# Kernel optimization log

Measured on AMD Instinct MI355X. Metric: run time of the kernel, lower is better.

## Reference

```python
import jax, jax.numpy as jnp
import numpy as np

ALPHA = 1.8   # Levy stability index (undefined global in source; chosen heavy-tailed)
BETA = 0.0    # symmetric
SIGMA = 0.5
DEPTH = 25
DIM = 64
HID = 100
BATCH = 262144


def _levy_noise(u_raw, w_raw):
    """Chambers-Mallows-Stuck sampler for symmetric alpha-stable (beta=0).
    u_raw, w_raw ~ U(0,1); returns clipped noise, scale=0.1, clamp [-10,10]."""
    U = jnp.pi * (u_raw - 0.5)                       # U(-pi/2, pi/2)
    W = -jnp.log(jnp.clip(w_raw, 1e-12, 1.0))        # Exp(1)
    inv_a = 1.0 / ALPHA
    X = (jnp.sin(ALPHA * U) / jnp.cos(U) ** inv_a) * \
        (jnp.cos(U - ALPHA * U) / jnp.clip(W, 1e-12, None)) ** ((1.0 - ALPHA) * inv_a)
    return jnp.clip(0.1 * X, -10.0, 10.0)


def setup_inputs() -> dict:
    key = jax.random.key(0)
    ks = jax.random.split(key, 8)
    d, h = DIM, HID
    return {
        "x": jax.random.normal(ks[0], (BATCH, d), dtype=jnp.float32),
        "u_raw": jax.random.uniform(ks[1], (DEPTH, d), dtype=jnp.float32),
        "w_raw": jax.random.uniform(ks[2], (DEPTH, d), dtype=jnp.float32),
        "W_down": jax.random.normal(ks[3], (d, d), dtype=jnp.float32) / np.sqrt(d),
        "b_down": jnp.zeros((d,), jnp.float32),
        "W_drift": jax.random.normal(ks[4], (d, d), dtype=jnp.float32) / np.sqrt(d),
        "b_drift": jnp.zeros((d,), jnp.float32),
        "W1": jax.random.normal(ks[5], (d, h), dtype=jnp.float32) / np.sqrt(d),
        "b1": jnp.zeros((h,), jnp.float32),
        "W2": jax.random.normal(ks[6], (h, 1), dtype=jnp.float32) / np.sqrt(h),
        "b2": jnp.zeros((1,), jnp.float32),
    }


def reference(x, u_raw, w_raw, W_down, b_down, W_drift, b_drift, W1, b1, W2, b2):
    dt = 1.0 / DEPTH
    out = x @ W_down + b_down                                   # [B, d]
    # diffusion logit on the INITIAL state, held fixed through the loop
    logit = jax.nn.relu(out @ W1 + b1) @ W2 + b2                # [B, 1]
    scale = SIGMA * jax.nn.sigmoid(logit) * dt ** (1.0 / ALPHA)  # [B, 1]
    noise = _levy_noise(u_raw, w_raw)                           # [DEPTH, d]

    def step(out, n):
        drift = jax.nn.relu(out @ W_drift + b_drift) + out      # DriftNet: relu(lin)+x
        return out + drift * dt + scale * n, None

    out, _ = jax.lax.scan(step, out, noise)
    drift_out = jax.nn.relu(out @ W_drift + b_drift) + out
    return drift_out, out
```

## Files before the change

### kernel.cpp

```cpp
#include <hip/hip_runtime.h>

#define DEPTH 25
#define DIM   64
#define HID   100

typedef _Float16 f16x4 __attribute__((ext_vector_type(4)));
typedef _Float16 f16x8 __attribute__((ext_vector_type(8)));
typedef __fp16   h2    __attribute__((ext_vector_type(2)));
typedef float    f32x4 __attribute__((ext_vector_type(4)));
typedef float    f32x2 __attribute__((ext_vector_type(2)));

__global__ __launch_bounds__(64) void levy_noise_kernel(
    const float* __restrict__ u_raw, const float* __restrict__ w_raw,
    float* __restrict__ noise)
{
    const int idx = blockIdx.x * 64 + threadIdx.x;
    if (idx >= DEPTH * DIM) return;
    float u = u_raw[idx];
    float w = w_raw[idx];
    float U  = 3.14159265358979323846f * (u - 0.5f);
    float Wv = -logf(fminf(fmaxf(w, 1e-12f), 1.0f));
    float t1 = sinf(1.8f * U) / powf(cosf(U), 0.5555555555555556f);
    float ratio = cosf(0.8f * U) / fmaxf(Wv, 1e-12f);
    float X = t1 * powf(ratio, -0.4444444444444444f);
    noise[idx] = fminf(fmaxf(0.1f * X, -10.0f), 10.0f);
}

__global__ __launch_bounds__(256) void preconv_kernel(
    const float* __restrict__ W_down, const float* __restrict__ W_drift,
    const float* __restrict__ W1,     const float* __restrict__ b1,
    const float* __restrict__ W2,
    _Float16* __restrict__ wpre, float* __restrict__ b1p, float* __restrict__ w2p)
{
    const int idx = blockIdx.x * 256 + threadIdx.x;
    if (idx < 7680) {
        int rel, kind;
        if (idx < 2048)      { kind = 0; rel = idx; }
        else if (idx < 4096) { kind = 1; rel = idx - 2048; }
        else                 { kind = 2; rel = idx - 4096; }
        const int fi    = rel >> 8;
        const int lane2 = (rel >> 2) & 63;
        const int j     = (rel & 3) * 2;
        const int m     = (fi >> 1) * 16 + (lane2 & 15);
        const int k     = (fi & 1) * 32 + ((j & 4) ? 16 : 0)
                        + (lane2 >> 4) * 4 + (j & 3);
        float v0, v1;
        if (kind == 0) {
            v0 = W_down[k * DIM + m];           v1 = W_down[(k + 1) * DIM + m];
        } else if (kind == 1) {
            v0 = 0.04f * W_drift[k * DIM + m];  v1 = 0.04f * W_drift[(k + 1) * DIM + m];
        } else {
            v0 = (m < HID) ? W1[k * HID + m] : 0.0f;
            v1 = (m < HID) ? W1[(k + 1) * HID + m] : 0.0f;
        }
        *(h2*)(wpre + idx * 2) = __builtin_amdgcn_cvt_pkrtz(v0, v1);
    } else if (idx < 7792) {
        const int i = idx - 7680;
        b1p[i] = (i < HID) ? b1[i] : 0.0f;
    } else if (idx < 7904) {
        const int i = idx - 7792;
        w2p[i] = (i < HID) ? W2[i] : 0.0f;
    }
}

union frag_u { h2 p[4]; f16x8 v; };

__global__ __launch_bounds__(256, 4) void sdenet_fused_pre(
    const float* __restrict__ x,      const float* __restrict__ noise_g,
    const _Float16* __restrict__ wpre,
    const float* __restrict__ b_down, const float* __restrict__ b_drift,
    const float* __restrict__ b1p,    const float* __restrict__ w2p,
    const float* __restrict__ b2,
    float* __restrict__ out, int batch)
{
    __shared__ float noise_lds[DEPTH * DIM];

    const int tid  = threadIdx.x;
    const int wave = tid >> 6;
    const int lane = tid & 63;
    const int r    = lane & 15;
    const int g    = lane >> 4;
    const int row  = blockIdx.x * 64 + wave * 16 + r;
    const int fbase = lane * 8;
    const float dt = 0.04f;

    {
        const float4* src = (const float4*)noise_g;
        float4* dst = (float4*)noise_lds;
        dst[tid] = src[tid];
        if (tid < 144) dst[tid + 256] = src[tid + 256];
    }
    float4 xlo[2], xhi[2];
    #pragma unroll
    for (int kt = 0; kt < 2; ++kt) {
        xlo[kt] = *(const float4*)(x + row * DIM + kt * 32 + g * 4);
        xhi[kt] = *(const float4*)(x + row * DIM + kt * 32 + 16 + g * 4);
    }
    __syncthreads();

    f16x8 bfrag[2];
    #pragma unroll
    for (int kt = 0; kt < 2; ++kt) {
        frag_u u;
        u.p[0] = __builtin_amdgcn_cvt_pkrtz(xlo[kt].x, xlo[kt].y);
        u.p[1] = __builtin_amdgcn_cvt_pkrtz(xlo[kt].z, xlo[kt].w);
        u.p[2] = __builtin_amdgcn_cvt_pkrtz(xhi[kt].x, xhi[kt].y);
        u.p[3] = __builtin_amdgcn_cvt_pkrtz(xhi[kt].z, xhi[kt].w);
        bfrag[kt] = u.v;
    }

    f32x2 out2[4][2];
    #pragma unroll
    for (int Mt = 0; Mt < 4; ++Mt) {
        f32x4 acc = *(const f32x4*)(b_down + Mt * 16 + g * 4);
        #pragma unroll
        for (int kt = 0; kt < 2; ++kt)
            acc = __builtin_amdgcn_mfma_f32_16x16x32_f16(
                *(const f16x8*)(wpre + (Mt * 2 + kt) * 512 + fbase),
                bfrag[kt], acc, 0, 0, 0);
        out2[Mt][0][0] = acc[0]; out2[Mt][0][1] = acc[1];
        out2[Mt][1][0] = acc[2]; out2[Mt][1][1] = acc[3];
    }

    auto refresh = [&]() {
        #pragma unroll
        for (int kt = 0; kt < 2; ++kt) {
            frag_u u;
            u.p[0] = __builtin_amdgcn_cvt_pkrtz(out2[2*kt  ][0][0], out2[2*kt  ][0][1]);
            u.p[1] = __builtin_amdgcn_cvt_pkrtz(out2[2*kt  ][1][0], out2[2*kt  ][1][1]);
            u.p[2] = __builtin_amdgcn_cvt_pkrtz(out2[2*kt+1][0][0], out2[2*kt+1][0][1]);
            u.p[3] = __builtin_amdgcn_cvt_pkrtz(out2[2*kt+1][1][0], out2[2*kt+1][1][1]);
            bfrag[kt] = u.v;
        }
    };
    refresh();

    const _Float16* w1pre = wpre + 8192;
    float partial = 0.0f;
    #pragma unroll
    for (int Mt = 0; Mt < 7; ++Mt) {
        f32x4 acc = *(const f32x4*)(b1p + Mt * 16 + g * 4);
        #pragma unroll
        for (int kt = 0; kt < 2; ++kt)
            acc = __builtin_amdgcn_mfma_f32_16x16x32_f16(
                *(const f16x8*)(w1pre + (Mt * 2 + kt) * 512 + fbase),
                bfrag[kt], acc, 0, 0, 0);
        #pragma unroll
        for (int reg = 0; reg < 4; ++reg)
            partial += fmaxf(acc[reg], 0.0f) * w2p[Mt * 16 + g * 4 + reg];
    }
    partial += __shfl_xor(partial, 16);
    partial += __shfl_xor(partial, 32);
    const float logit = partial + b2[0];
    const float scale = 0.5f * (1.0f / (1.0f + expf(-logit)))
                      * powf(0.04f, 1.0f / 1.8f);
    const f32x2 scale2 = { scale, scale };
    const f32x2 c104   = { 1.04f, 1.04f };
    const f32x2 zero2  = { 0.0f, 0.0f };

    f16x8 aWd[4][2];
    #pragma unroll
    for (int Mt = 0; Mt < 4; ++Mt)
        #pragma unroll
        for (int kt = 0; kt < 2; ++kt)
            aWd[Mt][kt] = *(const f16x8*)(wpre + 4096 + (Mt * 2 + kt) * 512 + fbase);

    f32x4 biasd[4];
    #pragma unroll
    for (int Mt = 0; Mt < 4; ++Mt) {
        f32x4 b = *(const f32x4*)(b_drift + Mt * 16 + g * 4);
        biasd[Mt][0] = b[0] * dt; biasd[Mt][1] = b[1] * dt;
        biasd[Mt][2] = b[2] * dt; biasd[Mt][3] = b[3] * dt;
    }

    #pragma unroll
    for (int t = 0; t < DEPTH; ++t) {
        f32x4 nz[4];
        #pragma unroll
        for (int Mt = 0; Mt < 4; ++Mt)
            nz[Mt] = *(const f32x4*)(noise_lds + t * DIM + Mt * 16 + g * 4);

        f32x4 acc[4];
        #pragma unroll
        for (int Mt = 0; Mt < 4; ++Mt) {
            acc[Mt] = __builtin_amdgcn_mfma_f32_16x16x32_f16(
                aWd[Mt][0], bfrag[0], biasd[Mt], 0, 0, 0);
            acc[Mt] = __builtin_amdgcn_mfma_f32_16x16x32_f16(
                aWd[Mt][1], bfrag[1], acc[Mt], 0, 0, 0);
        }
        #pragma unroll
        for (int Mt = 0; Mt < 4; ++Mt) {
            #pragma unroll
            for (int h = 0; h < 2; ++h) {
                f32x2 a2 = { acc[Mt][2*h], acc[Mt][2*h+1] };
                f32x2 n2 = { nz[Mt][2*h],  nz[Mt][2*h+1] };
                f32x2 rel = __builtin_elementwise_max(a2, zero2);
                f32x2 tmp = __builtin_elementwise_fma(out2[Mt][h], c104, rel);
                out2[Mt][h] = __builtin_elementwise_fma(scale2, n2, tmp);
            }
        }
        refresh();
    }

    const long long out2_off = (long long)batch * DIM;
    #pragma unroll
    for (int Mt = 0; Mt < 4; ++Mt) {
        f32x4 acc = __builtin_amdgcn_mfma_f32_16x16x32_f16(
            aWd[Mt][0], bfrag[0], biasd[Mt], 0, 0, 0);
        acc = __builtin_amdgcn_mfma_f32_16x16x32_f16(
            aWd[Mt][1], bfrag[1], acc, 0, 0, 0);
        float o0 = out2[Mt][0][0], o1 = out2[Mt][0][1];
        float o2 = out2[Mt][1][0], o3 = out2[Mt][1][1];
        float4 dv, ov;
        dv.x = fmaf(fmaxf(acc[0], 0.0f), 25.0f, o0);
        dv.y = fmaf(fmaxf(acc[1], 0.0f), 25.0f, o1);
        dv.z = fmaf(fmaxf(acc[2], 0.0f), 25.0f, o2);
        dv.w = fmaf(fmaxf(acc[3], 0.0f), 25.0f, o3);
        ov.x = o0; ov.y = o1; ov.z = o2; ov.w = o3;
        *(float4*)(out + (long long)row * DIM + Mt * 16 + g * 4) = dv;
        *(float4*)(out + out2_off + (long long)row * DIM + Mt * 16 + g * 4) = ov;
    }
}

__global__ __launch_bounds__(256, 4) void sdenet_fused_fb(
    const float* __restrict__ x,      const float* __restrict__ noise_g,
    const float* __restrict__ W_down, const float* __restrict__ b_down,
    const float* __restrict__ W_drift,const float* __restrict__ b_drift,
    const float* __restrict__ W1,     const float* __restrict__ b1,
    const float* __restrict__ W2,     const float* __restrict__ b2,
    float* __restrict__ out, int batch)
{
    __shared__ float    noise_lds[DEPTH * DIM];
    __shared__ float    bias_lds[DIM];
    __shared__ _Float16 wdown[4096];
    __shared__ _Float16 wdrift[4096];
    __shared__ _Float16 w1buf[7168];

    const int tid  = threadIdx.x;
    const int wave = tid >> 6;
    const int lane = tid & 63;
    const int r    = lane & 15;
    const int g    = lane >> 4;
    const int row  = blockIdx.x * 64 + wave * 16 + r;
    const int fbase = lane * 8;
    const float dt = 0.04f;

    {
        const float4* src = (const float4*)noise_g;
        float4* dst = (float4*)noise_lds;
        #pragma unroll
        for (int it = 0; it < 2; ++it) {
            int idx = tid + it * 256;
            if (idx < DEPTH * DIM / 4) dst[idx] = src[idx];
        }
    }
    if (tid < DIM) bias_lds[tid] = dt * b_drift[tid];

    for (int idx2 = tid; idx2 < 2048; idx2 += 256) {
        const int fi    = idx2 >> 8;
        const int lane2 = (idx2 >> 2) & 63;
        const int j     = (idx2 & 3) * 2;
        const int m     = (fi >> 1) * 16 + (lane2 & 15);
        const int k     = (fi & 1) * 32 + ((j & 4) ? 16 : 0)
                        + (lane2 >> 4) * 4 + (j & 3);
        *(h2*)(wdown + idx2 * 2) =
            __builtin_amdgcn_cvt_pkrtz(W_down[k * DIM + m],
                                       W_down[(k + 1) * DIM + m]);
        *(h2*)(wdrift + idx2 * 2) =
            __builtin_amdgcn_cvt_pkrtz(dt * W_drift[k * DIM + m],
                                       dt * W_drift[(k + 1) * DIM + m]);
    }
    for (int idx2 = tid; idx2 < 3584; idx2 += 256) {
        const int fi    = idx2 >> 8;
        const int lane2 = (idx2 >> 2) & 63;
        const int j     = (idx2 & 3) * 2;
        const int n     = (fi >> 1) * 16 + (lane2 & 15);
        const int k     = (fi & 1) * 32 + ((j & 4) ? 16 : 0)
                        + (lane2 >> 4) * 4 + (j & 3);
        const float v0 = (n < HID) ? W1[k * HID + n] : 0.0f;
        const float v1 = (n < HID) ? W1[(k + 1) * HID + n] : 0.0f;
        *(h2*)(w1buf + idx2 * 2) = __builtin_amdgcn_cvt_pkrtz(v0, v1);
    }

    float4 xlo[2], xhi[2];
    #pragma unroll
    for (int kt = 0; kt < 2; ++kt) {
        xlo[kt] = *(const float4*)(x + row * DIM + kt * 32 + g * 4);
        xhi[kt] = *(const float4*)(x + row * DIM + kt * 32 + 16 + g * 4);
    }
    __syncthreads();

    f16x8 bfrag[2];
    #pragma unroll
    for (int kt = 0; kt < 2; ++kt) {
        frag_u u;
        u.p[0] = __builtin_amdgcn_cvt_pkrtz(xlo[kt].x, xlo[kt].y);
        u.p[1] = __builtin_amdgcn_cvt_pkrtz(xlo[kt].z, xlo[kt].w);
        u.p[2] = __builtin_amdgcn_cvt_pkrtz(xhi[kt].x, xhi[kt].y);
        u.p[3] = __builtin_amdgcn_cvt_pkrtz(xhi[kt].z, xhi[kt].w);
        bfrag[kt] = u.v;
    }

    f32x2 out2[4][2];
    #pragma unroll
    for (int Mt = 0; Mt < 4; ++Mt) {
        f32x4 acc = *(const f32x4*)(b_down + Mt * 16 + g * 4);
        #pragma unroll
        for (int kt = 0; kt < 2; ++kt)
            acc = __builtin_amdgcn_mfma_f32_16x16x32_f16(
                *(const f16x8*)(wdown + (Mt * 2 + kt) * 512 + fbase),
                bfrag[kt], acc, 0, 0, 0);
        out2[Mt][0][0] = acc[0]; out2[Mt][0][1] = acc[1];
        out2[Mt][1][0] = acc[2]; out2[Mt][1][1] = acc[3];
    }

    auto refresh = [&]() {
        #pragma unroll
        for (int kt = 0; kt < 2; ++kt) {
            frag_u u;
            u.p[0] = __builtin_amdgcn_cvt_pkrtz(out2[2*kt  ][0][0], out2[2*kt  ][0][1]);
            u.p[1] = __builtin_amdgcn_cvt_pkrtz(out2[2*kt  ][1][0], out2[2*kt  ][1][1]);
            u.p[2] = __builtin_amdgcn_cvt_pkrtz(out2[2*kt+1][0][0], out2[2*kt+1][0][1]);
            u.p[3] = __builtin_amdgcn_cvt_pkrtz(out2[2*kt+1][1][0], out2[2*kt+1][1][1]);
            bfrag[kt] = u.v;
        }
    };
    refresh();

    float partial = 0.0f;
    #pragma unroll
    for (int Mt = 0; Mt < 7; ++Mt) {
        f32x4 acc;
        #pragma unroll
        for (int reg = 0; reg < 4; ++reg) {
            const int n = Mt * 16 + g * 4 + reg;
            acc[reg] = (n < HID) ? b1[n] : 0.0f;
        }
        #pragma unroll
        for (int kt = 0; kt < 2; ++kt)
            acc = __builtin_amdgcn_mfma_f32_16x16x32_f16(
                *(const f16x8*)(w1buf + (Mt * 2 + kt) * 512 + fbase),
                bfrag[kt], acc, 0, 0, 0);
        #pragma unroll
        for (int reg = 0; reg < 4; ++reg) {
            const int n = Mt * 16 + g * 4 + reg;
            if (n < HID) partial += fmaxf(acc[reg], 0.0f) * W2[n];
        }
    }
    partial += __shfl_xor(partial, 16);
    partial += __shfl_xor(partial, 32);
    const float logit = partial + b2[0];
    const float scale = 0.5f * (1.0f / (1.0f + expf(-logit)))
                      * powf(0.04f, 1.0f / 1.8f);
    const f32x2 scale2 = { scale, scale };
    const f32x2 c104   = { 1.04f, 1.04f };
    const f32x2 zero2  = { 0.0f, 0.0f };

    f16x8 aWd[4][2];
    #pragma unroll
    for (int Mt = 0; Mt < 4; ++Mt)
        #pragma unroll
        for (int kt = 0; kt < 2; ++kt)
            aWd[Mt][kt] = *(const f16x8*)(wdrift + (Mt * 2 + kt) * 512 + fbase);

    #pragma unroll
    for (int t = 0; t < DEPTH; ++t) {
        f32x4 nz[4];
        #pragma unroll
        for (int Mt = 0; Mt < 4; ++Mt)
            nz[Mt] = *(const f32x4*)(noise_lds + t * DIM + Mt * 16 + g * 4);

        f32x4 acc[4];
        #pragma unroll
        for (int Mt = 0; Mt < 4; ++Mt) {
            acc[Mt] = *(const f32x4*)(bias_lds + Mt * 16 + g * 4);
            acc[Mt] = __builtin_amdgcn_mfma_f32_16x16x32_f16(
                aWd[Mt][0], bfrag[0], acc[Mt], 0, 0, 0);
            acc[Mt] = __builtin_amdgcn_mfma_f32_16x16x32_f16(
                aWd[Mt][1], bfrag[1], acc[Mt], 0, 0, 0);
        }
        #pragma unroll
        for (int Mt = 0; Mt < 4; ++Mt) {
            #pragma unroll
            for (int h = 0; h < 2; ++h) {
                f32x2 a2 = { acc[Mt][2*h], acc[Mt][2*h+1] };
                f32x2 n2 = { nz[Mt][2*h],  nz[Mt][2*h+1] };
                f32x2 rel = __builtin_elementwise_max(a2, zero2);
                f32x2 tmp = __builtin_elementwise_fma(out2[Mt][h], c104, rel);
                out2[Mt][h] = __builtin_elementwise_fma(scale2, n2, tmp);
            }
        }
        refresh();
    }

    const long long out2_off = (long long)batch * DIM;
    #pragma unroll
    for (int Mt = 0; Mt < 4; ++Mt) {
        f32x4 acc = *(const f32x4*)(bias_lds + Mt * 16 + g * 4);
        acc = __builtin_amdgcn_mfma_f32_16x16x32_f16(
            aWd[Mt][0], bfrag[0], acc, 0, 0, 0);
        acc = __builtin_amdgcn_mfma_f32_16x16x32_f16(
            aWd[Mt][1], bfrag[1], acc, 0, 0, 0);
        float o0 = out2[Mt][0][0], o1 = out2[Mt][0][1];
        float o2 = out2[Mt][1][0], o3 = out2[Mt][1][1];
        float4 dv, ov;
        dv.x = fmaf(fmaxf(acc[0], 0.0f), 25.0f, o0);
        dv.y = fmaf(fmaxf(acc[1], 0.0f), 25.0f, o1);
        dv.z = fmaf(fmaxf(acc[2], 0.0f), 25.0f, o2);
        dv.w = fmaf(fmaxf(acc[3], 0.0f), 25.0f, o3);
        ov.x = o0; ov.y = o1; ov.z = o2; ov.w = o3;
        *(float4*)(out + (long long)row * DIM + Mt * 16 + g * 4) = dv;
        *(float4*)(out + out2_off + (long long)row * DIM + Mt * 16 + g * 4) = ov;
    }
}

extern "C" void kernel_launch(void* const* d_in, const int* in_sizes, int n_in,
                              void* d_out, int out_size, void* d_ws, size_t ws_size,
                              hipStream_t stream) {
    const float* x       = (const float*)d_in[0];
    const float* u_raw   = (const float*)d_in[1];
    const float* w_raw   = (const float*)d_in[2];
    const float* W_down  = (const float*)d_in[3];
    const float* b_down  = (const float*)d_in[4];
    const float* W_drift = (const float*)d_in[5];
    const float* b_drift = (const float*)d_in[6];
    const float* W1      = (const float*)d_in[7];
    const float* b1      = (const float*)d_in[8];
    const float* W2      = (const float*)d_in[9];
    const float* b2      = (const float*)d_in[10];
    float* out   = (float*)d_out;

    float*     noise = (float*)d_ws;
    _Float16*  wpre  = (_Float16*)((char*)d_ws + 6400);
    float*     b1p   = (float*)((char*)d_ws + 37120);
    float*     w2p   = (float*)((char*)d_ws + 37568);

    const int batch = in_sizes[0] / DIM;
    const int blocks = batch / 64;

    levy_noise_kernel<<<DEPTH, 64, 0, stream>>>(u_raw, w_raw, noise);

    if (ws_size >= 38016) {
        preconv_kernel<<<31, 256, 0, stream>>>(W_down, W_drift, W1, b1, W2,
                                               wpre, b1p, w2p);
        sdenet_fused_pre<<<blocks, 256, 0, stream>>>(
            x, noise, wpre, b_down, b_drift, b1p, w2p, b2, out, batch);
    } else {
        sdenet_fused_fb<<<blocks, 256, 0, stream>>>(
            x, noise, W_down, b_down, W_drift, b_drift,
            W1, b1, W2, b2, out, batch);
    }
}
```

Baseline: 245.7 us.

## Process two row tiles per wave and merge noise and weight prep kernels

Each wave now handles 32 rows as two independent 16-row MFMA chains (A and B) that share the drift weight fragments and noise loads. The two interleaved chains are meant to hide MFMA latency in the serial 25-step recurrence, and the block covers 128 rows, so half as many blocks launch. The noise sampler and the weight pre-conversion are merged into one prep kernel to save a launch. In exchange, register pressure rises (launch bounds lowered to 3 waves per SIMD) and occupancy may drop.

Result: no change. 241.3 us (-1.8%).

```diff
diff --git a/kernel.cpp b/kernel.cpp
--- a/kernel.cpp
+++ b/kernel.cpp
@@ -10,34 +10,30 @@
 typedef float    f32x4 __attribute__((ext_vector_type(4)));
 typedef float    f32x2 __attribute__((ext_vector_type(2)));
 
-__global__ __launch_bounds__(64) void levy_noise_kernel(
-    const float* __restrict__ u_raw, const float* __restrict__ w_raw,
-    float* __restrict__ noise)
-{
-    const int idx = blockIdx.x * 64 + threadIdx.x;
-    if (idx >= DEPTH * DIM) return;
-    float u = u_raw[idx];
-    float w = w_raw[idx];
-    float U  = 3.14159265358979323846f * (u - 0.5f);
-    float Wv = -logf(fminf(fmaxf(w, 1e-12f), 1.0f));
-    float t1 = sinf(1.8f * U) / powf(cosf(U), 0.5555555555555556f);
-    float ratio = cosf(0.8f * U) / fmaxf(Wv, 1e-12f);
-    float X = t1 * powf(ratio, -0.4444444444444444f);
-    noise[idx] = fminf(fmaxf(0.1f * X, -10.0f), 10.0f);
-}
-
-__global__ __launch_bounds__(256) void preconv_kernel(
+__global__ __launch_bounds__(256) void prep_kernel(
+    const float* __restrict__ u_raw,  const float* __restrict__ w_raw,
     const float* __restrict__ W_down, const float* __restrict__ W_drift,
     const float* __restrict__ W1,     const float* __restrict__ b1,
     const float* __restrict__ W2,
-    _Float16* __restrict__ wpre, float* __restrict__ b1p, float* __restrict__ w2p)
+    float* __restrict__ noise, _Float16* __restrict__ wpre,
+    float* __restrict__ b1p, float* __restrict__ w2p)
 {
     const int idx = blockIdx.x * 256 + threadIdx.x;
-    if (idx < 7680) {
+    if (idx < DEPTH * DIM) {
+        float u = u_raw[idx];
+        float w = w_raw[idx];
+        float U  = 3.14159265358979323846f * (u - 0.5f);
+        float Wv = -logf(fminf(fmaxf(w, 1e-12f), 1.0f));
+        float t1 = sinf(1.8f * U) / powf(cosf(U), 0.5555555555555556f);
+        float ratio = cosf(0.8f * U) / fmaxf(Wv, 1e-12f);
+        float X = t1 * powf(ratio, -0.4444444444444444f);
+        noise[idx] = fminf(fmaxf(0.1f * X, -10.0f), 10.0f);
+    } else if (idx < 1600 + 7680) {
+        const int p = idx - 1600;
         int rel, kind;
-        if (idx < 2048)      { kind = 0; rel = idx; }
-        else if (idx < 4096) { kind = 1; rel = idx - 2048; }
-        else                 { kind = 2; rel = idx - 4096; }
+        if (p < 2048)      { kind = 0; rel = p; }
+        else if (p < 4096) { kind = 1; rel = p - 2048; }
+        else               { kind = 2; rel = p - 4096; }
         const int fi    = rel >> 8;
         const int lane2 = (rel >> 2) & 63;
         const int j     = (rel & 3) * 2;
@@ -53,19 +49,19 @@
             v0 = (m < HID) ? W1[k * HID + m] : 0.0f;
             v1 = (m < HID) ? W1[(k + 1) * HID + m] : 0.0f;
         }
-        *(h2*)(wpre + idx * 2) = __builtin_amdgcn_cvt_pkrtz(v0, v1);
-    } else if (idx < 7792) {
-        const int i = idx - 7680;
+        *(h2*)(wpre + p * 2) = __builtin_amdgcn_cvt_pkrtz(v0, v1);
+    } else if (idx < 9280 + 112) {
+        const int i = idx - 9280;
         b1p[i] = (i < HID) ? b1[i] : 0.0f;
-    } else if (idx < 7904) {
-        const int i = idx - 7792;
+    } else if (idx < 9392 + 112) {
+        const int i = idx - 9392;
         w2p[i] = (i < HID) ? W2[i] : 0.0f;
     }
 }
 
 union frag_u { h2 p[4]; f16x8 v; };
 
-__global__ __launch_bounds__(256, 4) void sdenet_fused_pre(
+__global__ __launch_bounds__(256, 3) void sdenet_fused_pre2(
     const float* __restrict__ x,      const float* __restrict__ noise_g,
     const _Float16* __restrict__ wpre,
     const float* __restrict__ b_down, const float* __restrict__ b_drift,
@@ -80,7 +76,9 @@
     const int lane = tid & 63;
     const int r    = lane & 15;
     const int g    = lane >> 4;
-    const int row  = blockIdx.x * 64 + wave * 16 + r;
+    const int base = blockIdx.x * 128 + wave * 32;
+    const int rowA = base + r;
+    const int rowB = base + 16 + r;
     const int fbase = lane * 8;
     const float dt = 0.04f;
 
@@ -90,73 +88,91 @@
         dst[tid] = src[tid];
         if (tid < 144) dst[tid + 256] = src[tid + 256];
     }
-    float4 xlo[2], xhi[2];
+    float4 xA[4], xB[4];
     #pragma unroll
     for (int kt = 0; kt < 2; ++kt) {
-        xlo[kt] = *(const float4*)(x + row * DIM + kt * 32 + g * 4);
-        xhi[kt] = *(const float4*)(x + row * DIM + kt * 32 + 16 + g * 4);
+        xA[2*kt]   = *(const float4*)(x + rowA * DIM + kt * 32 + g * 4);
+        xA[2*kt+1] = *(const float4*)(x + rowA * DIM + kt * 32 + 16 + g * 4);
+        xB[2*kt]   = *(const float4*)(x + rowB * DIM + kt * 32 + g * 4);
+        xB[2*kt+1] = *(const float4*)(x + rowB * DIM + kt * 32 + 16 + g * 4);
     }
     __syncthreads();
 
-    f16x8 bfrag[2];
+    f16x8 bfragA[2], bfragB[2];
     #pragma unroll
     for (int kt = 0; kt < 2; ++kt) {
-        frag_u u;
-        u.p[0] = __builtin_amdgcn_cvt_pkrtz(xlo[kt].x, xlo[kt].y);
-        u.p[1] = __builtin_amdgcn_cvt_pkrtz(xlo[kt].z, xlo[kt].w);
-        u.p[2] = __builtin_amdgcn_cvt_pkrtz(xhi[kt].x, xhi[kt].y);
-        u.p[3] = __builtin_amdgcn_cvt_pkrtz(xhi[kt].z, xhi[kt].w);
-        bfrag[kt] = u.v;
-    }
-
-    f32x2 out2[4][2];
+        frag_u ua, ub;
+        ua.p[0] = __builtin_amdgcn_cvt_pkrtz(xA[2*kt].x,   xA[2*kt].y);
+        ua.p[1] = __builtin_amdgcn_cvt_pkrtz(xA[2*kt].z,   xA[2*kt].w);
+        ua.p[2] = __builtin_amdgcn_cvt_pkrtz(xA[2*kt+1].x, xA[2*kt+1].y);
+        ua.p[3] = __builtin_amdgcn_cvt_pkrtz(xA[2*kt+1].z, xA[2*kt+1].w);
+        bfragA[kt] = ua.v;
+        ub.p[0] = __builtin_amdgcn_cvt_pkrtz(xB[2*kt].x,   xB[2*kt].y);
+        ub.p[1] = __builtin_amdgcn_cvt_pkrtz(xB[2*kt].z,   xB[2*kt].w);
+        ub.p[2] = __builtin_amdgcn_cvt_pkrtz(xB[2*kt+1].x, xB[2*kt+1].y);
+        ub.p[3] = __builtin_amdgcn_cvt_pkrtz(xB[2*kt+1].z, xB[2*kt+1].w);
+        bfragB[kt] = ub.v;
+    }
+
+    f32x2 outA[4][2], outB[4][2];
     #pragma unroll
     for (int Mt = 0; Mt < 4; ++Mt) {
-        f32x4 acc = *(const f32x4*)(b_down + Mt * 16 + g * 4);
-        #pragma unroll
-        for (int kt = 0; kt < 2; ++kt)
-            acc = __builtin_amdgcn_mfma_f32_16x16x32_f16(
-                *(const f16x8*)(wpre + (Mt * 2 + kt) * 512 + fbase),
-                bfrag[kt], acc, 0, 0, 0);
-        out2[Mt][0][0] = acc[0]; out2[Mt][0][1] = acc[1];
-        out2[Mt][1][0] = acc[2]; out2[Mt][1][1] = acc[3];
-    }
-
-    auto refresh = [&]() {
+        const f32x4 bd = *(const f32x4*)(b_down + Mt * 16 + g * 4);
+        f32x4 accA = bd, accB = bd;
+        #pragma unroll
+        for (int kt = 0; kt < 2; ++kt) {
+            const f16x8 wfrag = *(const f16x8*)(wpre + (Mt * 2 + kt) * 512 + fbase);
+            accA = __builtin_amdgcn_mfma_f32_16x16x32_f16(wfrag, bfragA[kt], accA, 0, 0, 0);
+            accB = __builtin_amdgcn_mfma_f32_16x16x32_f16(wfrag, bfragB[kt], accB, 0, 0, 0);
+        }
+        outA[Mt][0][0] = accA[0]; outA[Mt][0][1] = accA[1];
+        outA[Mt][1][0] = accA[2]; outA[Mt][1][1] = accA[3];
+        outB[Mt][0][0] = accB[0]; outB[Mt][0][1] = accB[1];
+        outB[Mt][1][0] = accB[2]; outB[Mt][1][1] = accB[3];
+    }
+
+    auto refreshg = [&](f32x2 (&o2)[4][2], f16x8 (&bf)[2]) {
         #pragma unroll
         for (int kt = 0; kt < 2; ++kt) {
             frag_u u;
-            u.p[0] = __builtin_amdgcn_cvt_pkrtz(out2[2*kt  ][0][0], out2[2*kt  ][0][1]);
-            u.p[1] = __builtin_amdgcn_cvt_pkrtz(out2[2*kt  ][1][0], out2[2*kt  ][1][1]);
-            u.p[2] = __builtin_amdgcn_cvt_pkrtz(out2[2*kt+1][0][0], out2[2*kt+1][0][1]);
-            u.p[3] = __builtin_amdgcn_cvt_pkrtz(out2[2*kt+1][1][0], out2[2*kt+1][1][1]);
-            bfrag[kt] = u.v;
+            u.p[0] = __builtin_amdgcn_cvt_pkrtz(o2[2*kt  ][0][0], o2[2*kt  ][0][1]);
+            u.p[1] = __builtin_amdgcn_cvt_pkrtz(o2[2*kt  ][1][0], o2[2*kt  ][1][1]);
+            u.p[2] = __builtin_amdgcn_cvt_pkrtz(o2[2*kt+1][0][0], o2[2*kt+1][0][1]);
+            u.p[3] = __builtin_amdgcn_cvt_pkrtz(o2[2*kt+1][1][0], o2[2*kt+1][1][1]);
+            bf[kt] = u.v;
         }
     };
-    refresh();
+    refreshg(outA, bfragA);
+    refreshg(outB, bfragB);
 
     const _Float16* w1pre = wpre + 8192;
-    float partial = 0.0f;
+    float partA = 0.0f, partB = 0.0f;
     #pragma unroll
     for (int Mt = 0; Mt < 7; ++Mt) {
-        f32x4 acc = *(const f32x4*)(b1p + Mt * 16 + g * 4);
-        #pragma unroll
-        for (int kt = 0; kt < 2; ++kt)
-            acc = __builtin_amdgcn_mfma_f32_16x16x32_f16(
-                *(const f16x8*)(w1pre + (Mt * 2 + kt) * 512 + fbase),
-                bfrag[kt], acc, 0, 0, 0);
-        #pragma unroll
-        for (int reg = 0; reg < 4; ++reg)
-            partial += fmaxf(acc[reg], 0.0f) * w2p[Mt * 16 + g * 4 + reg];
-    }
-    partial += __shfl_xor(partial, 16);
-    partial += __shfl_xor(partial, 32);
-    const float logit = partial + b2[0];
-    const float scale = 0.5f * (1.0f / (1.0f + expf(-logit)))
-                      * powf(0.04f, 1.0f / 1.8f);
-    const f32x2 scale2 = { scale, scale };
-    const f32x2 c104   = { 1.04f, 1.04f };
-    const f32x2 zero2  = { 0.0f, 0.0f };
+        const f32x4 b1v = *(const f32x4*)(b1p + Mt * 16 + g * 4);
+        f32x4 accA = b1v, accB = b1v;
+        #pragma unroll
+        for (int kt = 0; kt < 2; ++kt) {
+            const f16x8 wfrag = *(const f16x8*)(w1pre + (Mt * 2 + kt) * 512 + fbase);
+            accA = __builtin_amdgcn_mfma_f32_16x16x32_f16(wfrag, bfragA[kt], accA, 0, 0, 0);
+            accB = __builtin_amdgcn_mfma_f32_16x16x32_f16(wfrag, bfragB[kt], accB, 0, 0, 0);
+        }
+        #pragma unroll
+        for (int reg = 0; reg < 4; ++reg) {
+            const float w2v = w2p[Mt * 16 + g * 4 + reg];
+            partA += fmaxf(accA[reg], 0.0f) * w2v;
+            partB += fmaxf(accB[reg], 0.0f) * w2v;
+        }
+    }
+    partA += __shfl_xor(partA, 16); partA += __shfl_xor(partA, 32);
+    partB += __shfl_xor(partB, 16); partB += __shfl_xor(partB, 32);
+    const float sfac = 0.5f * powf(0.04f, 1.0f / 1.8f);
+    const float scaleA = sfac / (1.0f + expf(-(partA + b2[0])));
+    const float scaleB = sfac / (1.0f + expf(-(partB + b2[0])));
+    const f32x2 scA = { scaleA, scaleA };
+    const f32x2 scB = { scaleB, scaleB };
+    const f32x2 c104 = { 1.04f, 1.04f };
+    const f32x2 zero2 = { 0.0f, 0.0f };
 
     f16x8 aWd[4][2];
     #pragma unroll
@@ -173,52 +189,77 @@
         biasd[Mt][2] = b[2] * dt; biasd[Mt][3] = b[3] * dt;
     }
 
-    #pragma unroll
-    for (int t = 0; t < DEPTH; ++t) {
-        f32x4 nz[4];
-        #pragma unroll
-        for (int Mt = 0; Mt < 4; ++Mt)
-            nz[Mt] = *(const f32x4*)(noise_lds + t * DIM + Mt * 16 + g * 4);
-
-        f32x4 acc[4];
-        #pragma unroll
-        for (int Mt = 0; Mt < 4; ++Mt) {
-            acc[Mt] = __builtin_amdgcn_mfma_f32_16x16x32_f16(
-                aWd[Mt][0], bfrag[0], biasd[Mt], 0, 0, 0);
-            acc[Mt] = __builtin_amdgcn_mfma_f32_16x16x32_f16(
-                aWd[Mt][1], bfrag[1], acc[Mt], 0, 0, 0);
-        }
+    auto stepelt = [&](f32x2 (&o2)[4][2], f32x4 (&ac)[4], f32x4 (&nzv)[4],
+                       const f32x2& sc2) {
         #pragma unroll
         for (int Mt = 0; Mt < 4; ++Mt) {
             #pragma unroll
             for (int h = 0; h < 2; ++h) {
-                f32x2 a2 = { acc[Mt][2*h], acc[Mt][2*h+1] };
-                f32x2 n2 = { nz[Mt][2*h],  nz[Mt][2*h+1] };
+                f32x2 a2 = { ac[Mt][2*h], ac[Mt][2*h+1] };
+                f32x2 n2 = { nzv[Mt][2*h], nzv[Mt][2*h+1] };
                 f32x2 rel = __builtin_elementwise_max(a2, zero2);
-                f32x2 tmp = __builtin_elementwise_fma(out2[Mt][h], c104, rel);
-                out2[Mt][h] = __builtin_elementwise_fma(scale2, n2, tmp);
+                f32x2 tmp = __builtin_elementwise_fma(o2[Mt][h], c104, rel);
+                o2[Mt][h] = __builtin_elementwise_fma(sc2, n2, tmp);
             }
         }
-        refresh();
+    };
+
+    #pragma unroll 5
+    for (int t = 0; t < DEPTH; ++t) {
+        f32x4 nz[4];
+        #pragma unroll
+        for (int Mt = 0; Mt < 4; ++Mt)
+            nz[Mt] = *(const f32x4*)(noise_lds + t * DIM + Mt * 16 + g * 4);
+
+        f32x4 accA[4], accB[4];
+        #pragma unroll
+        for (int Mt = 0; Mt < 4; ++Mt) {
+            accA[Mt] = __builtin_amdgcn_mfma_f32_16x16x32_f16(
+                aWd[Mt][0], bfragA[0], biasd[Mt], 0, 0, 0);
+            accA[Mt] = __builtin_amdgcn_mfma_f32_16x16x32_f16(
+                aWd[Mt][1], bfragA[1], accA[Mt], 0, 0, 0);
+        }
+        #pragma unroll
+        for (int Mt = 0; Mt < 4; ++Mt) {
+            accB[Mt] = __builtin_amdgcn_mfma_f32_16x16x32_f16(
+                aWd[Mt][0], bfragB[0], biasd[Mt], 0, 0, 0);
+            accB[Mt] = __builtin_amdgcn_mfma_f32_16x16x32_f16(
+                aWd[Mt][1], bfragB[1], accB[Mt], 0, 0, 0);
+        }
+        stepelt(outA, accA, nz, scA);  refreshg(outA, bfragA);
+        stepelt(outB, accB, nz, scB);  refreshg(outB, bfragB);
     }
 
     const long long out2_off = (long long)batch * DIM;
     #pragma unroll
     for (int Mt = 0; Mt < 4; ++Mt) {
-        f32x4 acc = __builtin_amdgcn_mfma_f32_16x16x32_f16(
-            aWd[Mt][0], bfrag[0], biasd[Mt], 0, 0, 0);
-        acc = __builtin_amdgcn_mfma_f32_16x16x32_f16(
-            aWd[Mt][1], bfrag[1], acc, 0, 0, 0);
-        float o0 = out2[Mt][0][0], o1 = out2[Mt][0][1];
-        float o2 = out2[Mt][1][0], o3 = out2[Mt][1][1];
+        f32x4 accA = __builtin_amdgcn_mfma_f32_16x16x32_f16(
+            aWd[Mt][0], bfragA[0], biasd[Mt], 0, 0, 0);
+        accA = __builtin_amdgcn_mfma_f32_16x16x32_f16(
+            aWd[Mt][1], bfragA[1], accA, 0, 0, 0);
+        f32x4 accB = __builtin_amdgcn_mfma_f32_16x16x32_f16(
+            aWd[Mt][0], bfragB[0], biasd[Mt], 0, 0, 0);
+        accB = __builtin_amdgcn_mfma_f32_16x16x32_f16(
+            aWd[Mt][1], bfragB[1], accB, 0, 0, 0);
+
         float4 dv, ov;
-        dv.x = fmaf(fmaxf(acc[0], 0.0f), 25.0f, o0);
-        dv.y = fmaf(fmaxf(acc[1], 0.0f), 25.0f, o1);
-        dv.z = fmaf(fmaxf(acc[2], 0.0f), 25.0f, o2);
-        dv.w = fmaf(fmaxf(acc[3], 0.0f), 25.0f, o3);
-        ov.x = o0; ov.y = o1; ov.z = o2; ov.w = o3;
-        *(float4*)(out + (long long)row * DIM + Mt * 16 + g * 4) = dv;
-        *(float4*)(out + out2_off + (long long)row * DIM + Mt * 16 + g * 4) = ov;
+        ov.x = outA[Mt][0][0]; ov.y = outA[Mt][0][1];
+        ov.z = outA[Mt][1][0]; ov.w = outA[Mt][1][1];
+        dv.x = fmaf(fmaxf(accA[0], 0.0f), 25.0f, ov.x);
+        dv.y = fmaf(fmaxf(accA[1], 0.0f), 25.0f, ov.y);
+        dv.z = fmaf(fmaxf(accA[2], 0.0f), 25.0f, ov.z);
+        dv.w = fmaf(fmaxf(accA[3], 0.0f), 25.0f, ov.w);
+        *(float4*)(out + (long long)rowA * DIM + Mt * 16 + g * 4) = dv;
+        *(float4*)(out + out2_off + (long long)rowA * DIM + Mt * 16 + g * 4) = ov;
+
+        ov.x = outB[Mt][0][0]; ov.y = outB[Mt][0][1];
+        ov.z = outB[Mt][1][0]; ov.w = outB[Mt][1][1];
+        dv.x = fmaf(fmaxf(accB[0], 0.0f), 25.0f, ov.x);
+        dv.y = fmaf(fmaxf(accB[1], 0.0f), 25.0f, ov.y);
+        dv.z = fmaf(fmaxf(accB[2], 0.0f), 25.0f, ov.z);
+        dv.w = fmaf(fmaxf(accB[3], 0.0f), 25.0f, ov.w);
+        *(float4*)(out + (long long)rowB * DIM + Mt * 16 + g * 4) = dv;
+        *(float4*)(out + out2_off + (long long)rowB * DIM + Mt * 16 + g * 4) = ov;
     }
 }
 
@@ -436,17 +477,17 @@
     float*     w2p   = (float*)((char*)d_ws + 37568);
 
     const int batch = in_sizes[0] / DIM;
-    const int blocks = batch / 64;
-
-    levy_noise_kernel<<<DEPTH, 64, 0, stream>>>(u_raw, w_raw, noise);
 
     if (ws_size >= 38016) {
-        preconv_kernel<<<31, 256, 0, stream>>>(W_down, W_drift, W1, b1, W2,
-                                               wpre, b1p, w2p);
-        sdenet_fused_pre<<<blocks, 256, 0, stream>>>(
+        prep_kernel<<<38, 256, 0, stream>>>(u_raw, w_raw, W_down, W_drift,
+                                            W1, b1, W2, noise, wpre, b1p, w2p);
+        sdenet_fused_pre2<<<batch / 128, 256, 0, stream>>>(
             x, noise, wpre, b_down, b_drift, b1p, w2p, b2, out, batch);
     } else {
-        sdenet_fused_fb<<<blocks, 256, 0, stream>>>(
+        prep_kernel<<<7, 256, 0, stream>>>(u_raw, w_raw, W_down, W_drift,
+                                           W1, b1, W2, noise,
+                                           (_Float16*)noise, noise, noise);
+        sdenet_fused_fb<<<batch / 64, 256, 0, stream>>>(
             x, noise, W_down, b_down, W_drift, b_drift,
             W1, b1, W2, b2, out, batch);
     }
```

## Fuse prep kernels, use per-wave noise LDS copies, and interleave MFMA with the epilogue

Applied to the files above, without the earlier changes.

Merges the Levy noise kernel and the weight pre-conversion kernel into one launch, which removes a kernel launch. In the main kernel each wave now keeps its own copy of the noise table in LDS, so the block-wide __syncthreads is gone, and launch bounds are raised to 5 blocks per SM. The time-step loop is split into two halves: each half issues its MFMAs under raised s_setprio and then runs its element-wise update and fp16 repack, letting matrix and vector work overlap. In exchange, LDS per block grows fourfold, which may cap occupancy, and the tighter register budget risks spills.

Measured after the change: 262.8 us. +6.9%, slower.

```diff
diff --git a/kernel.cpp b/kernel.cpp
--- a/kernel.cpp
+++ b/kernel.cpp
@@ -10,34 +10,30 @@
 typedef float    f32x4 __attribute__((ext_vector_type(4)));
 typedef float    f32x2 __attribute__((ext_vector_type(2)));
 
-__global__ __launch_bounds__(64) void levy_noise_kernel(
-    const float* __restrict__ u_raw, const float* __restrict__ w_raw,
-    float* __restrict__ noise)
-{
-    const int idx = blockIdx.x * 64 + threadIdx.x;
-    if (idx >= DEPTH * DIM) return;
-    float u = u_raw[idx];
-    float w = w_raw[idx];
-    float U  = 3.14159265358979323846f * (u - 0.5f);
-    float Wv = -logf(fminf(fmaxf(w, 1e-12f), 1.0f));
-    float t1 = sinf(1.8f * U) / powf(cosf(U), 0.5555555555555556f);
-    float ratio = cosf(0.8f * U) / fmaxf(Wv, 1e-12f);
-    float X = t1 * powf(ratio, -0.4444444444444444f);
-    noise[idx] = fminf(fmaxf(0.1f * X, -10.0f), 10.0f);
-}
-
-__global__ __launch_bounds__(256) void preconv_kernel(
+__global__ __launch_bounds__(256) void prep_kernel(
+    const float* __restrict__ u_raw,  const float* __restrict__ w_raw,
     const float* __restrict__ W_down, const float* __restrict__ W_drift,
     const float* __restrict__ W1,     const float* __restrict__ b1,
     const float* __restrict__ W2,
-    _Float16* __restrict__ wpre, float* __restrict__ b1p, float* __restrict__ w2p)
+    float* __restrict__ noise, _Float16* __restrict__ wpre,
+    float* __restrict__ b1p, float* __restrict__ w2p)
 {
     const int idx = blockIdx.x * 256 + threadIdx.x;
-    if (idx < 7680) {
+    if (idx < DEPTH * DIM) {
+        float u = u_raw[idx];
+        float w = w_raw[idx];
+        float U  = 3.14159265358979323846f * (u - 0.5f);
+        float Wv = -logf(fminf(fmaxf(w, 1e-12f), 1.0f));
+        float t1 = sinf(1.8f * U) / powf(cosf(U), 0.5555555555555556f);
+        float ratio = cosf(0.8f * U) / fmaxf(Wv, 1e-12f);
+        float X = t1 * powf(ratio, -0.4444444444444444f);
+        noise[idx] = fminf(fmaxf(0.1f * X, -10.0f), 10.0f);
+    } else if (idx < 1600 + 7680) {
+        const int p = idx - 1600;
         int rel, kind;
-        if (idx < 2048)      { kind = 0; rel = idx; }
-        else if (idx < 4096) { kind = 1; rel = idx - 2048; }
-        else                 { kind = 2; rel = idx - 4096; }
+        if (p < 2048)      { kind = 0; rel = p; }
+        else if (p < 4096) { kind = 1; rel = p - 2048; }
+        else               { kind = 2; rel = p - 4096; }
         const int fi    = rel >> 8;
         const int lane2 = (rel >> 2) & 63;
         const int j     = (rel & 3) * 2;
@@ -53,19 +49,19 @@
             v0 = (m < HID) ? W1[k * HID + m] : 0.0f;
             v1 = (m < HID) ? W1[(k + 1) * HID + m] : 0.0f;
         }
-        *(h2*)(wpre + idx * 2) = __builtin_amdgcn_cvt_pkrtz(v0, v1);
-    } else if (idx < 7792) {
-        const int i = idx - 7680;
+        *(h2*)(wpre + p * 2) = __builtin_amdgcn_cvt_pkrtz(v0, v1);
+    } else if (idx < 9280 + 112) {
+        const int i = idx - 9280;
         b1p[i] = (i < HID) ? b1[i] : 0.0f;
-    } else if (idx < 7904) {
-        const int i = idx - 7792;
+    } else if (idx < 9392 + 112) {
+        const int i = idx - 9392;
         w2p[i] = (i < HID) ? W2[i] : 0.0f;
     }
 }
 
 union frag_u { h2 p[4]; f16x8 v; };
 
-__global__ __launch_bounds__(256, 4) void sdenet_fused_pre(
+__global__ __launch_bounds__(256, 5) void sdenet_fused_pre3(
     const float* __restrict__ x,      const float* __restrict__ noise_g,
     const _Float16* __restrict__ wpre,
     const float* __restrict__ b_down, const float* __restrict__ b_drift,
@@ -73,7 +69,7 @@
     const float* __restrict__ b2,
     float* __restrict__ out, int batch)
 {
-    __shared__ float noise_lds[DEPTH * DIM];
+    __shared__ float noise_lds[4 * DEPTH * DIM];
 
     const int tid  = threadIdx.x;
     const int wave = tid >> 6;
@@ -84,28 +80,32 @@
     const int fbase = lane * 8;
     const float dt = 0.04f;
 
+    float* nbase = noise_lds + wave * (DEPTH * DIM);
     {
         const float4* src = (const float4*)noise_g;
-        float4* dst = (float4*)noise_lds;
-        dst[tid] = src[tid];
-        if (tid < 144) dst[tid + 256] = src[tid + 256];
-    }
-    float4 xlo[2], xhi[2];
+        float4* dst = (float4*)nbase;
+        #pragma unroll
+        for (int it = 0; it < 7; ++it) {
+            const int idx = lane + it * 64;
+            if (idx < DEPTH * DIM / 4) dst[idx] = src[idx];
+        }
+    }
+
+    float4 xv[4];
     #pragma unroll
     for (int kt = 0; kt < 2; ++kt) {
-        xlo[kt] = *(const float4*)(x + row * DIM + kt * 32 + g * 4);
-        xhi[kt] = *(const float4*)(x + row * DIM + kt * 32 + 16 + g * 4);
-    }
-    __syncthreads();
+        xv[2*kt]   = *(const float4*)(x + row * DIM + kt * 32 + g * 4);
+        xv[2*kt+1] = *(const float4*)(x + row * DIM + kt * 32 + 16 + g * 4);
+    }
 
     f16x8 bfrag[2];
     #pragma unroll
     for (int kt = 0; kt < 2; ++kt) {
         frag_u u;
-        u.p[0] = __builtin_amdgcn_cvt_pkrtz(xlo[kt].x, xlo[kt].y);
-        u.p[1] = __builtin_amdgcn_cvt_pkrtz(xlo[kt].z, xlo[kt].w);
-        u.p[2] = __builtin_amdgcn_cvt_pkrtz(xhi[kt].x, xhi[kt].y);
-        u.p[3] = __builtin_amdgcn_cvt_pkrtz(xhi[kt].z, xhi[kt].w);
+        u.p[0] = __builtin_amdgcn_cvt_pkrtz(xv[2*kt].x,   xv[2*kt].y);
+        u.p[1] = __builtin_amdgcn_cvt_pkrtz(xv[2*kt].z,   xv[2*kt].w);
+        u.p[2] = __builtin_amdgcn_cvt_pkrtz(xv[2*kt+1].x, xv[2*kt+1].y);
+        u.p[3] = __builtin_amdgcn_cvt_pkrtz(xv[2*kt+1].z, xv[2*kt+1].w);
         bfrag[kt] = u.v;
     }
 
@@ -122,18 +122,15 @@
         out2[Mt][1][0] = acc[2]; out2[Mt][1][1] = acc[3];
     }
 
-    auto refresh = [&]() {
-        #pragma unroll
-        for (int kt = 0; kt < 2; ++kt) {
-            frag_u u;
-            u.p[0] = __builtin_amdgcn_cvt_pkrtz(out2[2*kt  ][0][0], out2[2*kt  ][0][1]);
-            u.p[1] = __builtin_amdgcn_cvt_pkrtz(out2[2*kt  ][1][0], out2[2*kt  ][1][1]);
-            u.p[2] = __builtin_amdgcn_cvt_pkrtz(out2[2*kt+1][0][0], out2[2*kt+1][0][1]);
-            u.p[3] = __builtin_amdgcn_cvt_pkrtz(out2[2*kt+1][1][0], out2[2*kt+1][1][1]);
-            bfrag[kt] = u.v;
-        }
-    };
-    refresh();
+    #pragma unroll
+    for (int kt = 0; kt < 2; ++kt) {
+        frag_u u;
+        u.p[0] = __builtin_amdgcn_cvt_pkrtz(out2[2*kt  ][0][0], out2[2*kt  ][0][1]);
+        u.p[1] = __builtin_amdgcn_cvt_pkrtz(out2[2*kt  ][1][0], out2[2*kt  ][1][1]);
+        u.p[2] = __builtin_amdgcn_cvt_pkrtz(out2[2*kt+1][0][0], out2[2*kt+1][0][1]);
+        u.p[3] = __builtin_amdgcn_cvt_pkrtz(out2[2*kt+1][1][0], out2[2*kt+1][1][1]);
+        bfrag[kt] = u.v;
+    }
 
     const _Float16* w1pre = wpre + 8192;
     float partial = 0.0f;
@@ -175,31 +172,49 @@
 
     #pragma unroll
     for (int t = 0; t < DEPTH; ++t) {
-        f32x4 nz[4];
-        #pragma unroll
-        for (int Mt = 0; Mt < 4; ++Mt)
-            nz[Mt] = *(const f32x4*)(noise_lds + t * DIM + Mt * 16 + g * 4);
-
-        f32x4 acc[4];
-        #pragma unroll
-        for (int Mt = 0; Mt < 4; ++Mt) {
-            acc[Mt] = __builtin_amdgcn_mfma_f32_16x16x32_f16(
-                aWd[Mt][0], bfrag[0], biasd[Mt], 0, 0, 0);
-            acc[Mt] = __builtin_amdgcn_mfma_f32_16x16x32_f16(
-                aWd[Mt][1], bfrag[1], acc[Mt], 0, 0, 0);
-        }
-        #pragma unroll
-        for (int Mt = 0; Mt < 4; ++Mt) {
+        f16x8 nb[2];
+        #pragma unroll
+        for (int p = 0; p < 2; ++p) {
+            const int M0 = 2 * p, M1 = 2 * p + 1;
+            const f32x4 nz0 = *(const f32x4*)(nbase + t * DIM + M0 * 16 + g * 4);
+            const f32x4 nz1 = *(const f32x4*)(nbase + t * DIM + M1 * 16 + g * 4);
+
+            __builtin_amdgcn_s_setprio(1);
+            f32x4 a0 = __builtin_amdgcn_mfma_f32_16x16x32_f16(
+                aWd[M0][0], bfrag[0], biasd[M0], 0, 0, 0);
+            a0 = __builtin_amdgcn_mfma_f32_16x16x32_f16(
+                aWd[M0][1], bfrag[1], a0, 0, 0, 0);
+            f32x4 a1 = __builtin_amdgcn_mfma_f32_16x16x32_f16(
+                aWd[M1][0], bfrag[0], biasd[M1], 0, 0, 0);
+            a1 = __builtin_amdgcn_mfma_f32_16x16x32_f16(
+                aWd[M1][1], bfrag[1], a1, 0, 0, 0);
+            __builtin_amdgcn_s_setprio(0);
+
             #pragma unroll
             for (int h = 0; h < 2; ++h) {
-                f32x2 a2 = { acc[Mt][2*h], acc[Mt][2*h+1] };
-                f32x2 n2 = { nz[Mt][2*h],  nz[Mt][2*h+1] };
+                f32x2 a2 = { a0[2*h], a0[2*h+1] };
+                f32x2 n2 = { nz0[2*h], nz0[2*h+1] };
                 f32x2 rel = __builtin_elementwise_max(a2, zero2);
-                f32x2 tmp = __builtin_elementwise_fma(out2[Mt][h], c104, rel);
-                out2[Mt][h] = __builtin_elementwise_fma(scale2, n2, tmp);
+                f32x2 tmp = __builtin_elementwise_fma(out2[M0][h], c104, rel);
+                out2[M0][h] = __builtin_elementwise_fma(scale2, n2, tmp);
             }
-        }
-        refresh();
+            #pragma unroll
+            for (int h = 0; h < 2; ++h) {
+                f32x2 a2 = { a1[2*h], a1[2*h+1] };
+                f32x2 n2 = { nz1[2*h], nz1[2*h+1] };
+                f32x2 rel = __builtin_elementwise_max(a2, zero2);
+                f32x2 tmp = __builtin_elementwise_fma(out2[M1][h], c104, rel);
+                out2[M1][h] = __builtin_elementwise_fma(scale2, n2, tmp);
+            }
+            frag_u u;
+            u.p[0] = __builtin_amdgcn_cvt_pkrtz(out2[M0][0][0], out2[M0][0][1]);
+            u.p[1] = __builtin_amdgcn_cvt_pkrtz(out2[M0][1][0], out2[M0][1][1]);
+            u.p[2] = __builtin_amdgcn_cvt_pkrtz(out2[M1][0][0], out2[M1][0][1]);
+            u.p[3] = __builtin_amdgcn_cvt_pkrtz(out2[M1][1][0], out2[M1][1][1]);
+            nb[p] = u.v;
+        }
+        bfrag[0] = nb[0];
+        bfrag[1] = nb[1];
     }
 
     const long long out2_off = (long long)batch * DIM;
@@ -436,17 +451,17 @@
     float*     w2p   = (float*)((char*)d_ws + 37568);
 
     const int batch = in_sizes[0] / DIM;
-    const int blocks = batch / 64;
-
-    levy_noise_kernel<<<DEPTH, 64, 0, stream>>>(u_raw, w_raw, noise);
 
     if (ws_size >= 38016) {
-        preconv_kernel<<<31, 256, 0, stream>>>(W_down, W_drift, W1, b1, W2,
-                                               wpre, b1p, w2p);
-        sdenet_fused_pre<<<blocks, 256, 0, stream>>>(
+        prep_kernel<<<38, 256, 0, stream>>>(u_raw, w_raw, W_down, W_drift,
+                                            W1, b1, W2, noise, wpre, b1p, w2p);
+        sdenet_fused_pre3<<<batch / 64, 256, 0, stream>>>(
             x, noise, wpre, b_down, b_drift, b1p, w2p, b2, out, batch);
     } else {
-        sdenet_fused_fb<<<blocks, 256, 0, stream>>>(
+        prep_kernel<<<7, 256, 0, stream>>>(u_raw, w_raw, W_down, W_drift,
+                                           W1, b1, W2, noise,
+                                           (_Float16*)noise, noise, noise);
+        sdenet_fused_fb<<<batch / 64, 256, 0, stream>>>(
             x, noise, W_down, b_down, W_drift, b_drift,
             W1, b1, W2, b2, out, batch);
     }
```
